# Kernel tuning notes

Measured on AMD Instinct MI355X. Metric: run time of the kernel, lower is better.

The kernel has to match this reference:

```python
import jax, jax.numpy as jnp
import numpy as np
import math

B, H, N, L = 8, 512, 64, 2048


def setup_inputs() -> dict:
    key = jax.random.key(0)
    k_u, k_c, k_dt, k_d, k_w, k_b, k_ar, k_ai = jax.random.split(key, 8)
    u = jax.random.normal(k_u, (B, H, L), dtype=jnp.float32)
    # C ~ complex randn, stored as (..., 2) real/imag pairs (torch.view_as_real)
    C_ri = jax.random.normal(k_c, (H, N, 2), dtype=jnp.float32)
    # log_dt ~ Uniform(log(dt_min), log(dt_max))
    lo, hi = math.log(0.001), math.log(0.1)
    log_dt = jax.random.uniform(k_dt, (H,), dtype=jnp.float32) * (hi - lo) + lo
    D = jax.random.normal(k_d, (H,), dtype=jnp.float32)
    # Conv1d(H, 2H, kernel_size=1) -> weight (2H, H), bias (2H), kaiming-ish scale
    W = jax.random.normal(k_w, (2 * H, H), dtype=jnp.float32) / math.sqrt(H)
    b = jax.random.normal(k_b, (2 * H,), dtype=jnp.float32) * 0.01
    # Fixed diagonal state matrix A: Re(A) uniform in [-0.9, -0.8), Im(A) random
    a_re = -0.9 + 0.1 * jax.random.uniform(k_ar, (N,), dtype=jnp.float32)
    a_im = math.pi * jnp.arange(N, dtype=jnp.float32)  # stable oscillation freqs
    A_ri = jnp.stack([a_re, a_im], axis=-1)
    return {"u": u, "C_ri": C_ri, "log_dt": log_dt, "D": D, "W": W, "b": b, "A_ri": A_ri}


def _forward(u, C_ri, log_dt, D, W, b, A_ri):
    Lseq = u.shape[-1]
    C = C_ri[..., 0] + 1j * C_ri[..., 1]          # (H, N) complex
    A = A_ri[..., 0] + 1j * A_ri[..., 1]          # (N,) complex
    dt = jnp.exp(log_dt)                           # (H,)
    dtA = dt[:, None] * A[None, :]                 # (H, N)
    # Vandermonde: exp(dtA * l) for l in [0, L)  -> (H, N, L) complex
    K = jnp.exp(dtA[:, :, None] * jnp.arange(Lseq, dtype=jnp.float32))
    Ct = C * (jnp.exp(dtA) - 1.0) / A              # (H, N)
    k = 2.0 * jnp.einsum('hn,hnl->hl', Ct, K).real  # (H, L) real kernel
    # FFT long convolution (linear conv via length-2L circular conv)
    nfft = 2 * Lseq
    y = jnp.fft.irfft(jnp.fft.rfft(u, n=nfft) * jnp.fft.rfft(k, n=nfft), n=nfft)[..., :Lseq]
    y = y + D[:, None] * u                         # skip connection
    y = jax.nn.gelu(y, approximate=False)          # torch nn.GELU default = exact erf
    # Conv1d kernel_size=1 == per-position linear, then GLU over channel dim
    z = jnp.einsum('oh,bhl->bol', W, y) + b[:, None]  # (B, 2H, L)
    a, g = jnp.split(z, 2, axis=-2)
    return a * jax.nn.sigmoid(g)                   # (B, H, L)


def reference(u, C_ri, log_dt, D, W, b, A_ri):
    return _forward(u, C_ri, log_dt, D, W, b, A_ri)
```

## Files before the change

kernel.cpp:

```cpp
#include <hip/hip_runtime.h>
#include <math.h>

#define Hh 512
#define Nn 64
#define Ll 2048
#define Bb 8

typedef float f32x4 __attribute__((ext_vector_type(4)));
typedef __bf16 bf16x8 __attribute__((ext_vector_type(8)));

__device__ __forceinline__ unsigned short f2b(float x) {
  unsigned u = __builtin_bit_cast(unsigned, x);
  u += 0x7FFFu + ((u >> 16) & 1u);
  return (unsigned short)(u >> 16);
}
__device__ __forceinline__ float b2f(unsigned short b) {
  unsigned u = ((unsigned)b) << 16;
  return __builtin_bit_cast(float, u);
}

union BF8 {
  unsigned short us[8];
  bf16x8 v;
  uint4 q;
};

__device__ __forceinline__ uint4 cvt8q(const float* p) {
  float4 a = *(const float4*)p;
  float4 b = *(const float4*)(p + 4);
  BF8 o;
  o.us[0] = f2b(a.x); o.us[1] = f2b(a.y); o.us[2] = f2b(a.z); o.us[3] = f2b(a.w);
  o.us[4] = f2b(b.x); o.us[5] = f2b(b.y); o.us[6] = f2b(b.z); o.us[7] = f2b(b.w);
  return o.q;
}

__device__ __forceinline__ float gelu_f(float y) {
  float t = y * y;
  float p = y * fmaf(0.0713548162726f, t, 1.59576912161f);
  float e = __expf(-p);
  return y / (1.0f + e);
}

__global__ __launch_bounds__(512) void prep_kernel(
    const float* __restrict__ C_ri, const float* __restrict__ log_dt,
    const float* __restrict__ A_ri, const float* __restrict__ W,
    unsigned short* __restrict__ A1, unsigned short* __restrict__ A2,
    float* __restrict__ lamQ, unsigned short* __restrict__ Wimg) {
  int tid = threadIdx.x;
  if (blockIdx.x >= 512) {
    int id = (blockIdx.x - 512) * 512 + tid;
    int slot = id & 3, row = (id >> 2) & 127, kt = (id >> 9) & 15, ot = id >> 13;
    int o = (row < 64) ? (ot * 64 + row) : (512 + ot * 64 + row - 64);
    uint4 v = cvt8q(W + (size_t)o * 512 + kt * 32 + slot * 8);
    int sp = slot ^ ((row >> 1) & 3);
    *(uint4*)((char*)Wimg + (((size_t)ot * 16 + kt) * 8192) + row * 64 + sp * 16) = v;
    return;
  }
  __shared__ char sm[49152];
  __shared__ float kqs[64];
  __shared__ float kpart[8][64];
  float* kt = (float*)sm;
  char* A1s = sm;
  char* A2s = sm + 16384;
  int h = blockIdx.x;
  int n = tid & 63, part = tid >> 6;

  float dt = expf(log_dt[h]);
  float ar = A_ri[2 * n], ai = A_ri[2 * n + 1];
  float er = expf(dt * ar);
  float sn, cs;
  sincosf(dt * ai, &sn, &cs);
  float lr = er * cs, li = er * sn;
  float em1r = lr - 1.0f, em1i = li;
  float cr = C_ri[(h * 64 + n) * 2], ci = C_ri[(h * 64 + n) * 2 + 1];
  float numr = cr * em1r - ci * em1i;
  float numi = cr * em1i + ci * em1r;
  float den = ar * ar + ai * ai;
  float ctr = (numr * ar + numi * ai) / den;
  float cti = (numi * ar - numr * ai) / den;
  float l8r = lr, l8i = li;
#pragma unroll
  for (int s = 0; s < 3; ++s) {
    float t = l8r * l8r - l8i * l8i;
    l8i = 2.0f * l8r * l8i;
    l8r = t;
  }
  if (part == 0) {
    float qr = l8r, qi = l8i;
#pragma unroll
    for (int s = 0; s < 3; ++s) {
      float t = qr * qr - qi * qi;
      qi = 2.0f * qr * qi;
      qr = t;
    }
    lamQ[h * 128 + 2 * n] = qr;
    lamQ[h * 128 + 2 * n + 1] = qi;
  }
  float lpr = 1.0f, lpi = 0.0f;
  for (int s = 0; s < part; ++s) {
    float t = lpr * l8r - lpi * l8i;
    lpi = lpr * l8i + lpi * l8r;
    lpr = t;
  }
  int e0 = part * 8;
  {
    float vr = ctr * lpr - cti * lpi, vi = ctr * lpi + cti * lpr;
#pragma unroll
    for (int j = 0; j < 8; ++j) {
      kt[(e0 + j) * 64 + n] = vr;
      float t = vr * lr - vi * li;
      vi = vr * li + vi * lr;
      vr = t;
    }
  }
  __syncthreads();
  {
    float s = 0.0f;
#pragma unroll
    for (int j = 0; j < 8; ++j) s += kt[n * 64 + ((e0 + j + n) & 63)];
    kpart[part][n] = s;
  }
  __syncthreads();
  if (part == 0) {
    float s = 0.0f;
#pragma unroll
    for (int p2 = 0; p2 < 8; ++p2) s += kpart[p2][n];
    kqs[n] = 2.0f * s;
  }
  __syncthreads();
  {
    BF8 R0, I0;
    float vr = lpr, vi = lpi;
#pragma unroll
    for (int j = 0; j < 8; ++j) {
      int idx = 7 - j;
      R0.us[idx] = f2b(vr);
      I0.us[idx] = f2b(vi);
      float t = vr * lr - vi * li;
      vi = vr * li + vi * lr;
      vr = t;
    }
    int qlo = 56 - e0;
    int rowR = 2 * n, rowI = 2 * n + 1;
    *(uint4*)(A1s + ((rowR * 128 + 2 * qlo) ^ ((rowR & 7) << 4))) = R0.q;
    *(uint4*)(A1s + ((rowI * 128 + 2 * qlo) ^ ((rowI & 7) << 4))) = I0.q;
  }
  {
    float c1r = ctr * lr - cti * li, c1i = ctr * li + cti * lr;
    float wr = 2.0f * (c1r * lpr - c1i * lpi);
    float wi = 2.0f * (c1r * lpi + c1i * lpr);
#pragma unroll
    for (int j = 0; j < 8; ++j) {
      int t = e0 + j;
      *(unsigned*)(A2s + ((t * 512 + 128 + 4 * n) ^ ((t & 7) << 4))) =
          (unsigned)f2b(wr) | ((unsigned)f2b(-wi) << 16);
      float tm = wr * lr - wi * li;
      wi = wr * li + wi * lr;
      wr = tm;
    }
  }
  {
    int tau = n;
    BF8 o;
#pragma unroll
    for (int j = 0; j < 8; ++j) {
      int q = e0 + j;
      o.us[j] = (q <= tau) ? f2b(kqs[tau - q]) : (unsigned short)0;
    }
    *(uint4*)(A2s + ((tau * 512 + 2 * e0) ^ ((tau & 7) << 4))) = o.q;
  }
  __syncthreads();
#pragma unroll
  for (int i = 0; i < 2; ++i) {
    int byte = (i * 512 + tid) * 16;
    int row = byte >> 7;
    *(uint4*)((char*)A1 + (size_t)h * 16384 + byte) =
        *(const uint4*)(A1s + (byte ^ ((row & 7) << 4)));
  }
#pragma unroll
  for (int i = 0; i < 4; ++i) {
    int idx = i * 512 + tid;
    int row = idx >> 5;
    int byte = row * 512 + (idx & 31) * 16;
    *(uint4*)((char*)A2 + (size_t)h * 32768 + byte) =
        *(const uint4*)(A2s + (byte ^ ((row & 7) << 4)));
  }
}

__global__ __launch_bounds__(256, 5) void fused_conv_kernel(
    const float* __restrict__ u, const unsigned short* __restrict__ A1,
    const unsigned short* __restrict__ A2, const float* __restrict__ lamQ,
    const float* __restrict__ Dv, unsigned short* __restrict__ gy) {
  __shared__ char SXb[16384];
  __shared__ char Ub[8192];
  __shared__ float2 sX16[2][64];
  int h = blockIdx.x;
  int bs = blockIdx.y * 2;
  int tid = threadIdx.x;
  int w = tid >> 6, lane = tid & 63, lg = lane >> 4, l15 = lane & 15;

  {
    int row = tid >> 2, k0 = (tid & 3) * 16;
    int b = bs + (row >> 5), c = row & 31;
    const float* up = u + ((size_t)(b * Hh + h)) * Ll + c * 64 + k0;
    uint4 v0 = cvt8q(up), v1 = cvt8q(up + 8);
    int base = row * 128 + k0 * 2;
    int swz = (row & 7) << 4;
    *(uint4*)(Ub + (base ^ swz)) = v0;
    *(uint4*)(Ub + ((base + 16) ^ swz)) = v1;
  }
  bf16x8 a1f[2][2];
#pragma unroll
  for (int i = 0; i < 2; ++i) {
    int row = (2 * w + i) * 16 + l15;
#pragma unroll
    for (int kb = 0; kb < 2; ++kb)
      a1f[i][kb] = *(const bf16x8*)(A1 + ((size_t)h * 128 + row) * 64 + kb * 32 + lg * 8);
  }
  __syncthreads();

#pragma unroll
  for (int ct = 0; ct < 4; ++ct) {
    int bc = ct * 16 + l15;
    bf16x8 bu[2];
#pragma unroll
    for (int kb = 0; kb < 2; ++kb)
      bu[kb] = *(const bf16x8*)(Ub + ((bc * 128 + kb * 64 + lg * 16) ^ ((bc & 7) << 4)));
#pragma unroll
    for (int i = 0; i < 2; ++i) {
      f32x4 acc = {0.f, 0.f, 0.f, 0.f};
      acc = __builtin_amdgcn_mfma_f32_16x16x32_bf16(a1f[i][0], bu[0], acc, 0, 0, 0);
      acc = __builtin_amdgcn_mfma_f32_16x16x32_bf16(a1f[i][1], bu[1], acc, 0, 0, 0);
      int n2q = (2 * w + i) * 16 + lg * 4;
      uint2 pk;
      pk.x = f2b(acc[0]) | ((unsigned)f2b(acc[1]) << 16);
      pk.y = f2b(acc[2]) | ((unsigned)f2b(acc[3]) << 16);
      *(uint2*)(SXb + ((bc * 256 + n2q * 2) ^ ((bc & 7) << 4))) = pk;
    }
  }
  __syncthreads();

  bf16x8 a2f[6];
  int rowA = w * 16 + l15;
#pragma unroll
  for (int kb = 0; kb < 6; ++kb)
    a2f[kb] = *(const bf16x8*)(A2 + ((size_t)h * 64 + rowA) * 256 + kb * 32 + lg * 8);

  int nn = tid & 63, bpart = tid >> 6;
  int rbloc = bpart >> 1, rhalf = bpart & 1;
  float lqr = lamQ[h * 128 + 2 * nn], lqi = lamQ[h * 128 + 2 * nn + 1];
  {
    float Xr = 0.f, Xi = 0.f;
    int cbase = rbloc * 32 + rhalf * 16;
    for (int c = 0; c < 16; ++c) {
      int bc = cbase + c;
      int byte = (bc * 256 + 4 * nn) ^ ((bc & 7) << 4);
      unsigned ps = *(const unsigned*)(SXb + byte);
      *(unsigned*)(SXb + byte) = (unsigned)f2b(Xr) | ((unsigned)f2b(Xi) << 16);
      float Sr = b2f((unsigned short)(ps & 0xFFFF));
      float Si = b2f((unsigned short)(ps >> 16));
      float nXr = lqr * Xr - lqi * Xi + Sr;
      float nXi = lqr * Xi + lqi * Xr + Si;
      Xr = nXr;
      Xi = nXi;
    }
    if (rhalf == 0) sX16[rbloc][nn] = make_float2(Xr, Xi);
  }
  __syncthreads();
  if (rhalf) {
    float2 x16 = sX16[rbloc][nn];
    float cr = x16.x, ci = x16.y;
    int cbase = rbloc * 32 + 16;
#pragma unroll
    for (int c = 0; c < 16; ++c) {
      int bc = cbase + c;
      int byte = (bc * 256 + 4 * nn) ^ ((bc & 7) << 4);
      unsigned pv = *(const unsigned*)(SXb + byte);
      float vr = b2f((unsigned short)(pv & 0xFFFF)) + cr;
      float vi = b2f((unsigned short)(pv >> 16)) + ci;
      *(unsigned*)(SXb + byte) = (unsigned)f2b(vr) | ((unsigned)f2b(vi) << 16);
      float t = cr * lqr - ci * lqi;
      ci = cr * lqi + ci * lqr;
      cr = t;
    }
  }
  __syncthreads();

  float Dh = Dv[h];
  int t0 = w * 16 + lg * 4;
  f32x4 acc4[4];
  uint2 usk[4];
#pragma unroll
  for (int ct = 0; ct < 4; ++ct) {
    int bc = ct * 16 + l15;
    f32x4 acc = {0.f, 0.f, 0.f, 0.f};
#pragma unroll
    for (int kb = 0; kb < 2; ++kb) {
      bf16x8 bu = *(const bf16x8*)(Ub + ((bc * 128 + kb * 64 + lg * 16) ^ ((bc & 7) << 4)));
      acc = __builtin_amdgcn_mfma_f32_16x16x32_bf16(a2f[kb], bu, acc, 0, 0, 0);
    }
#pragma unroll
    for (int kb = 2; kb < 6; ++kb) {
      bf16x8 bx = *(const bf16x8*)(SXb + ((bc * 256 + ((kb - 2) * 32 + lg * 8) * 2) ^ ((bc & 7) << 4)));
      acc = __builtin_amdgcn_mfma_f32_16x16x32_bf16(a2f[kb], bx, acc, 0, 0, 0);
    }
    acc4[ct] = acc;
    usk[ct] = *(const uint2*)(Ub + ((bc * 128 + t0 * 2) ^ ((bc & 7) << 4)));
  }
  __syncthreads();

#pragma unroll
  for (int ct = 0; ct < 4; ++ct) {
    int bc = ct * 16 + l15;
    const unsigned short* up = (const unsigned short*)&usk[ct];
    unsigned short e[4];
#pragma unroll
    for (int r = 0; r < 4; ++r) {
      float y = fmaf(Dh, b2f(up[r]), acc4[ct][r]);
      e[r] = f2b(gelu_f(y));
    }
    uint2 pk;
    pk.x = e[0] | ((unsigned)e[1] << 16);
    pk.y = e[2] | ((unsigned)e[3] << 16);
    *(uint2*)(Ub + ((bc * 128 + t0 * 2) ^ ((bc & 7) << 4))) = pk;
  }
  __syncthreads();

#pragma unroll
  for (int i = 0; i < 2; ++i) {
    int j = tid + 256 * i;
    int row = j >> 3, q = j & 7;
    int byte = row * 128 + q * 16;
    uint4 v = *(const uint4*)(Ub + (byte ^ ((row & 7) << 4)));
    int b = bs + (row >> 5), c = row & 31;
    *(uint4*)(gy + ((size_t)(b * Hh + h)) * Ll + c * 64 + q * 8) = v;
  }
}

__global__ __launch_bounds__(256, 3) void glu_kernel(
    const unsigned short* __restrict__ Wimg, const unsigned short* __restrict__ gy,
    const float* __restrict__ bias, float* __restrict__ out) {
  __shared__ char sA[2][8192];
  __shared__ char sB[2][8192];
  int lt = blockIdx.x;
  int ot = blockIdx.y;
  int b = lt >> 4, lseg = lt & 15;
  int t = threadIdx.x;
  int lane = t & 63, lg = lane >> 4, l15 = lane & 15;
  int w = t >> 6, wm = w >> 1, wn = w & 1;
  int p = t >> 4, cg = t & 15;
  const char* Abase = (const char*)Wimg + (size_t)ot * 131072;
  const unsigned short* gybase = gy + (size_t)b * Hh * Ll + lseg * 128 + cg * 8 + 2 * p * Ll;

  int offA[2], offG[2];
#pragma unroll
  for (int mt = 0; mt < 2; ++mt) {
    int rA = wm * 32 + mt * 16 + l15;
    offA[mt] = rA * 64 + ((lg ^ ((rA >> 1) & 3)) << 4);
    int rG = rA + 64;
    offG[mt] = rG * 64 + ((lg ^ ((rG >> 1) & 3)) << 4);
  }
  int offB[4];
#pragma unroll
  for (int nt = 0; nt < 4; ++nt) {
    int rB = wn * 64 + nt * 16 + l15;
    int pr = ((rB >> 3) << 3) | ((rB & 7) ^ ((rB >> 3) & 7));
    offB[nt] = (lg << 11) + (pr << 4);
  }
  int offW[8];
#pragma unroll
  for (int j = 0; j < 8; ++j) {
    int pr = (cg << 3) | (j ^ (cg & 7));
    offW[j] = ((p >> 2) << 11) + (pr << 4) + ((p & 3) << 2);
  }

  f32x4 accA[2][4], accG[2][4];
#pragma unroll
  for (int mt = 0; mt < 2; ++mt)
#pragma unroll
    for (int nt = 0; nt < 4; ++nt) {
      accA[mt][nt] = (f32x4){0.f, 0.f, 0.f, 0.f};
      accG[mt][nt] = (f32x4){0.f, 0.f, 0.f, 0.f};
    }

  {
    const char* ga = Abase + t * 16;
    __builtin_amdgcn_global_load_lds(ga, (char*)&sA[0][0] + t * 16, 16, 0, 0);
    __builtin_amdgcn_global_load_lds(ga + 4096, (char*)&sA[0][0] + 4096 + t * 16, 16, 0, 0);
    BF8 r0, r1;
    r0.q = *(const uint4*)gybase;
    r1.q = *(const uint4*)(gybase + Ll);
#pragma unroll
    for (int j = 0; j < 8; ++j)
      *(unsigned*)(&sB[0][0] + offW[j]) =
          (unsigned)r0.us[j] | ((unsigned)r1.us[j] << 16);
  }
  __syncthreads();

  for (int kt = 0; kt < 16; ++kt) {
    int cur = kt & 1;
    BF8 r0, r1;
    if (kt < 15) {
      const char* ga = Abase + (kt + 1) * 8192 + t * 16;
      char* da = (char*)&sA[cur ^ 1][0] + t * 16;
      __builtin_amdgcn_global_load_lds(ga, da, 16, 0, 0);
      __builtin_amdgcn_global_load_lds(ga + 4096, da + 4096, 16, 0, 0);
      r0.q = *(const uint4*)(gybase + (size_t)(kt + 1) * 32 * Ll);
      r1.q = *(const uint4*)(gybase + (size_t)(kt + 1) * 32 * Ll + Ll);
    }
    const char* bufA = &sA[cur][0];
    const char* bufB = &sB[cur][0];
    bf16x8 aA[2], aG[2], bB[4];
#pragma unroll
    for (int mt = 0; mt < 2; ++mt) {
      aA[mt] = *(const bf16x8*)(bufA + offA[mt]);
      aG[mt] = *(const bf16x8*)(bufA + offG[mt]);
    }
#pragma unroll
    for (int nt = 0; nt < 4; ++nt)
      bB[nt] = *(const bf16x8*)(bufB + offB[nt]);
#pragma unroll
    for (int mt = 0; mt < 2; ++mt)
#pragma unroll
      for (int nt = 0; nt < 4; ++nt) {
        accA[mt][nt] = __builtin_amdgcn_mfma_f32_16x16x32_bf16(bB[nt], aA[mt], accA[mt][nt], 0, 0, 0);
        accG[mt][nt] = __builtin_amdgcn_mfma_f32_16x16x32_bf16(bB[nt], aG[mt], accG[mt][nt], 0, 0, 0);
      }
    if (kt < 15) {
      char* db = &sB[cur ^ 1][0];
#pragma unroll
      for (int j = 0; j < 8; ++j)
        *(unsigned*)(db + offW[j]) =
            (unsigned)r0.us[j] | ((unsigned)r1.us[j] << 16);
    }
    __syncthreads();
  }

#pragma unroll
  for (int mt = 0; mt < 2; ++mt) {
    int oA = ot * 64 + wm * 32 + mt * 16 + l15;
    float ba = bias[oA];
    float bg = bias[512 + oA];
    float* orow = out + ((size_t)(b * Hh) + oA) * Ll + lseg * 128 + wn * 64 + lg * 4;
#pragma unroll
    for (int nt = 0; nt < 4; ++nt) {
      float4 res;
      float* rp = (float*)&res;
#pragma unroll
      for (int r = 0; r < 4; ++r) {
        float a = accA[mt][nt][r] + ba;
        float g = accG[mt][nt][r] + bg;
        rp[r] = a * (1.0f / (1.0f + __expf(-g)));
      }
      *(float4*)(orow + nt * 16) = res;
    }
  }
}

extern "C" void kernel_launch(void* const* d_in, const int* in_sizes, int n_in,
                              void* d_out, int out_size, void* d_ws,
                              size_t ws_size, hipStream_t stream) {
  const float* u      = (const float*)d_in[0];
  const float* C_ri   = (const float*)d_in[1];
  const float* log_dt = (const float*)d_in[2];
  const float* Dv     = (const float*)d_in[3];
  const float* W      = (const float*)d_in[4];
  const float* bias   = (const float*)d_in[5];
  const float* A_ri   = (const float*)d_in[6];
  float* out = (float*)d_out;

  char* ws = (char*)d_ws;
  unsigned short* A1   = (unsigned short*)ws;
  unsigned short* A2   = (unsigned short*)(ws + 8388608);
  float*          lamQ = (float*)(ws + 25165824);
  unsigned short* Wimg = (unsigned short*)(ws + 25427968);
  unsigned short* gy   = (unsigned short*)(ws + 26476544);

  prep_kernel<<<640, 512, 0, stream>>>(C_ri, log_dt, A_ri, W, A1, A2, lamQ, Wimg);
  fused_conv_kernel<<<dim3(Hh, 4), 256, 0, stream>>>(u, A1, A2, lamQ, Dv, gy);
  glu_kernel<<<dim3(128, 8), 256, 0, stream>>>(Wimg, gy, bias, out);
}
```

Baseline: 60.13 us.

## Share each gy tile across two output tiles in 512-thread GLU blocks

```diff
diff --git a/kernel.cpp b/kernel.cpp
--- a/kernel.cpp
+++ b/kernel.cpp
@@ -337,19 +337,24 @@
   }
 }
 
-__global__ __launch_bounds__(256, 3) void glu_kernel(
+__global__ __launch_bounds__(512, 4) void glu_kernel(
     const unsigned short* __restrict__ Wimg, const unsigned short* __restrict__ gy,
     const float* __restrict__ bias, float* __restrict__ out) {
-  __shared__ char sA[2][8192];
+  __shared__ char sA[2][2][8192];
   __shared__ char sB[2][8192];
   int lt = blockIdx.x;
-  int ot = blockIdx.y;
+  int oz = blockIdx.y;
   int b = lt >> 4, lseg = lt & 15;
   int t = threadIdx.x;
   int lane = t & 63, lg = lane >> 4, l15 = lane & 15;
-  int w = t >> 6, wm = w >> 1, wn = w & 1;
-  int p = t >> 4, cg = t & 15;
-  const char* Abase = (const char*)Wimg + (size_t)ot * 131072;
+  int w = t >> 6;
+  int otl = w & 1;
+  int ot = oz * 2 + otl;
+  int wm = (w >> 2) & 1, wn = (w >> 1) & 1;
+  int doB = (t < 256);
+  int p = (t >> 4) & 15, cg = t & 15;
+  const char* Abase0 = (const char*)Wimg + (size_t)(oz * 2) * 131072;
+  const char* Abase1 = (const char*)Wimg + (size_t)(oz * 2 + 1) * 131072;
   const unsigned short* gybase = gy + (size_t)b * Hh * Ll + lseg * 128 + cg * 8 + 2 * p * Ll;
 
   int offA[2], offG[2];
@@ -384,16 +389,17 @@
     }
 
   {
-    const char* ga = Abase + t * 16;
-    __builtin_amdgcn_global_load_lds(ga, (char*)&sA[0][0] + t * 16, 16, 0, 0);
-    __builtin_amdgcn_global_load_lds(ga + 4096, (char*)&sA[0][0] + 4096 + t * 16, 16, 0, 0);
-    BF8 r0, r1;
-    r0.q = *(const uint4*)gybase;
-    r1.q = *(const uint4*)(gybase + Ll);
-#pragma unroll
-    for (int j = 0; j < 8; ++j)
-      *(unsigned*)(&sB[0][0] + offW[j]) =
-          (unsigned)r0.us[j] | ((unsigned)r1.us[j] << 16);
+    __builtin_amdgcn_global_load_lds(Abase0 + t * 16, (char*)&sA[0][0][0] + t * 16, 16, 0, 0);
+    __builtin_amdgcn_global_load_lds(Abase1 + t * 16, (char*)&sA[0][1][0] + t * 16, 16, 0, 0);
+    if (doB) {
+      BF8 r0, r1;
+      r0.q = *(const uint4*)gybase;
+      r1.q = *(const uint4*)(gybase + Ll);
+#pragma unroll
+      for (int j = 0; j < 8; ++j)
+        *(unsigned*)(&sB[0][0] + offW[j]) =
+            (unsigned)r0.us[j] | ((unsigned)r1.us[j] << 16);
+    }
   }
   __syncthreads();
 
@@ -401,14 +407,16 @@
     int cur = kt & 1;
     BF8 r0, r1;
     if (kt < 15) {
-      const char* ga = Abase + (kt + 1) * 8192 + t * 16;
-      char* da = (char*)&sA[cur ^ 1][0] + t * 16;
-      __builtin_amdgcn_global_load_lds(ga, da, 16, 0, 0);
-      __builtin_amdgcn_global_load_lds(ga + 4096, da + 4096, 16, 0, 0);
-      r0.q = *(const uint4*)(gybase + (size_t)(kt + 1) * 32 * Ll);
-      r1.q = *(const uint4*)(gybase + (size_t)(kt + 1) * 32 * Ll + Ll);
-    }
-    const char* bufA = &sA[cur][0];
+      __builtin_amdgcn_global_load_lds(Abase0 + (kt + 1) * 8192 + t * 16,
+                                       (char*)&sA[cur ^ 1][0][0] + t * 16, 16, 0, 0);
+      __builtin_amdgcn_global_load_lds(Abase1 + (kt + 1) * 8192 + t * 16,
+                                       (char*)&sA[cur ^ 1][1][0] + t * 16, 16, 0, 0);
+      if (doB) {
+        r0.q = *(const uint4*)(gybase + (size_t)(kt + 1) * 32 * Ll);
+        r1.q = *(const uint4*)(gybase + (size_t)(kt + 1) * 32 * Ll + Ll);
+      }
+    }
+    const char* bufA = &sA[cur][otl][0];
     const char* bufB = &sB[cur][0];
     bf16x8 aA[2], aG[2], bB[4];
 #pragma unroll
@@ -426,7 +434,7 @@
         accA[mt][nt] = __builtin_amdgcn_mfma_f32_16x16x32_bf16(bB[nt], aA[mt], accA[mt][nt], 0, 0, 0);
         accG[mt][nt] = __builtin_amdgcn_mfma_f32_16x16x32_bf16(bB[nt], aG[mt], accG[mt][nt], 0, 0, 0);
       }
-    if (kt < 15) {
+    if (kt < 15 && doB) {
       char* db = &sB[cur ^ 1][0];
 #pragma unroll
       for (int j = 0; j < 8; ++j)
@@ -478,5 +486,5 @@
 
   prep_kernel<<<640, 512, 0, stream>>>(C_ri, log_dt, A_ri, W, A1, A2, lamQ, Wimg);
   fused_conv_kernel<<<dim3(Hh, 4), 256, 0, stream>>>(u, A1, A2, lamQ, Dv, gy);
-  glu_kernel<<<dim3(128, 8), 256, 0, stream>>>(Wimg, gy, bias, out);
-}
+  glu_kernel<<<dim3(128, 4), 512, 0, stream>>>(Wimg, gy, bias, out);
+}
```

Measured after the change: 59.73 us. About the same (-0.7%).
